# Kernel optimization log

Hardware: AMD Instinct MI355X
Metric: run time of the kernel (lower is better)

Reference implementation:

```python
import math
import jax, jax.numpy as jnp
import numpy as np
from jax import lax

MUL = 16           # multiplicity of 0e and 1o in input and output irreps
NRB = 8            # num_radial_basis
DIAMETER = 3.0
STEPS = (1.0, 1.0, 1.0)
DIM = 4 * MUL      # 16 scalars + 16 vectors * 3 = 64 channels


def _constants():
    # lattice from __init__: arange(-s, s+1) * step per axis, s = floor(r/step)
    r = DIAMETER / 2
    axes = [np.arange(-math.floor(r / st), math.floor(r / st) + 1.0) * st for st in STEPS]
    lattice = np.stack(np.meshgrid(*axes, indexing='ij'), axis=-1)  # [Kx,Ky,Kz,3]
    d = np.linalg.norm(lattice, axis=-1)                            # [Kx,Ky,Kz]
    # soft_one_hot_linspace(basis='smooth_finite', cutoff=True)
    values = np.linspace(0.0, r, NRB + 2)[1:-1]
    step = values[1] - values[0]
    diff = (d[..., None] - values) / step
    inside = diff ** 2 < 1.0
    emb = np.where(inside, 1.14136 * np.exp(2.0) * np.exp(-2.0 / np.where(inside, 1.0 - diff ** 2, 1.0)), 0.0)
    # spherical harmonics, normalize=True, normalization='component'
    n = lattice / np.maximum(d[..., None], 1e-12)  # unit vectors; 0 at the origin voxel
    sh0 = np.ones_like(d)                          # Y_0 (component normalized)
    sh1 = np.sqrt(3.0) * n                         # Y_1 (component normalized)
    return emb.astype(np.float32), sh0.astype(np.float32), sh1.astype(np.float32)

EMB, SH0, SH1 = _constants()
KX, KY, KZ = SH0.shape  # 3,3,3


def setup_inputs() -> dict:
    key = jax.random.key(0)
    ks = jax.random.split(key, 7)
    B, G = 4, 32
    return {
        'x': jax.random.normal(ks[0], (B, G, G, G, DIM), jnp.float32),
        'W_sc0': jax.random.normal(ks[1], (MUL, MUL), jnp.float32),  # Linear 0e->0e
        'W_sc1': jax.random.normal(ks[2], (MUL, MUL), jnp.float32),  # Linear 1o->1o
        'w1': jax.random.normal(ks[3], (NRB, MUL, MUL), jnp.float32),  # path 0e x 0e -> 0e
        'w2': jax.random.normal(ks[4], (NRB, MUL, MUL), jnp.float32),  # path 0e x 1o -> 1o
        'w3': jax.random.normal(ks[5], (NRB, MUL, MUL), jnp.float32),  # path 1o x 0e -> 1o
        'w4': jax.random.normal(ks[6], (NRB, MUL, MUL), jnp.float32),  # path 1o x 1o -> 0e
    }


def _kernel(w1, w2, w3, w4):
    # radial basis -> per-voxel path weights, divided by kernel volume (as in source)
    emb, sh0, sh1 = jnp.asarray(EMB), jnp.asarray(SH0), jnp.asarray(SH1)
    norm = float(KX * KY * KZ)
    W1, W2, W3, W4 = [jnp.einsum('xyzk,kio->xyzio', emb, w) / norm for w in (w1, w2, w3, w4)]
    # path normalization: each output irrep receives 2 paths of fan_in mul*1 = 16 -> 1/sqrt(32)
    alpha = 1.0 / np.sqrt(2.0 * MUL)
    # tp.right blocks (Clebsch-Gordan contractions, lmax=1):
    k00 = alpha * W1 * sh0[..., None, None]                                              # [.,i,o]
    k01 = alpha * jnp.einsum('xyzio,xyzm->xyziom', W2, sh1).reshape(KX, KY, KZ, MUL, 3 * MUL)
    k10 = (alpha / np.sqrt(3.0)) * jnp.einsum('xyzio,xyzm->xyzimo', W4, sh1).reshape(KX, KY, KZ, 3 * MUL, MUL)
    k11 = alpha * jnp.einsum('xyzio,mn->xyzimon', W3 * sh0[..., None, None],
                             jnp.eye(3, dtype=W3.dtype)).reshape(KX, KY, KZ, 3 * MUL, 3 * MUL)
    return jnp.concatenate([jnp.concatenate([k00, k01], axis=-1),
                            jnp.concatenate([k10, k11], axis=-1)], axis=-2)  # [Kx,Ky,Kz,64,64]


def reference(x, W_sc0, W_sc1, w1, w2, w3, w4):
    B, X, Y, Z, _ = x.shape
    inv_sqrt_mul = 1.0 / np.sqrt(MUL)
    # self-connection: e3nn Linear per irrep (applied pointwise over b,x,y,z)
    xs = x[..., :MUL]                                   # [B,X,Y,Z,16] scalars
    xv = x[..., MUL:].reshape(B, X, Y, Z, MUL, 3)       # [B,X,Y,Z,16,3] vectors
    sc_s = (xs @ W_sc0) * inv_sqrt_mul
    sc_v = jnp.einsum('bxyzic,io->bxyzoc', xv, W_sc1) * inv_sqrt_mul
    sc = jnp.concatenate([sc_s, sc_v.reshape(B, X, Y, Z, 3 * MUL)], axis=-1)
    # position-dependent equivariant kernel + standard 3D conv
    k = _kernel(w1, w2, w3, w4)
    conv = lax.conv_general_dilated(x, k, (1, 1, 1), 'SAME',
                                    dimension_numbers=('NXYZC', 'XYZIO', 'NXYZC'))
    return sc + conv
```

## Files before the change

### kernel.cpp

```cpp
#include <hip/hip_runtime.h>

typedef unsigned short u16;
typedef unsigned int u32;
typedef __bf16 bf16x8 __attribute__((ext_vector_type(8)));
typedef float f32x4 __attribute__((ext_vector_type(4)));
typedef u32 u32x4 __attribute__((ext_vector_type(4)));

#define AS1 __attribute__((address_space(1)))
#define AS3 __attribute__((address_space(3)))

__device__ __align__(16) u16 g_kT[27 * 64 * 64];
__device__ __align__(16) u16 g_kTr[27 * 8 * 512];

__device__ __forceinline__ u16 f2bf(float f) {
    unsigned int u = __float_as_uint(f);
    u += 0x7FFFu + ((u >> 16) & 1u);
    return (u16)(u >> 16);
}

__device__ __forceinline__ u32 pack_bf(float a, float b) {
    u32 ua = __float_as_uint(a) + 0x8000u;
    u32 ub = __float_as_uint(b) + 0x8000u;
    return __builtin_amdgcn_perm(ub, ua, 0x07060302u);
}

__global__ __launch_bounds__(256) void prep(
    const float* __restrict__ Wsc0, const float* __restrict__ Wsc1,
    const float* __restrict__ w1, const float* __restrict__ w2,
    const float* __restrict__ w3, const float* __restrict__ w4,
    const float* __restrict__ x, u16* __restrict__ xb, u32* __restrict__ zp)
{
    const int tid = threadIdx.x;
    if (blockIdx.x < 27) {
        if (tid >= 64) return;
        const int t = blockIdx.x;
        const int c = tid;
        const int dx = t / 9 - 1, dy = (t / 3) % 3 - 1, dz = t % 3 - 1;
        const float d = sqrtf((float)(dx * dx + dy * dy + dz * dz));
        const float step = 1.5f / 9.0f;
        float emb[8];
#pragma unroll
        for (int k = 0; k < 8; ++k) {
            float diff = (d - (float)(k + 1) * step) / step;
            float q = diff * diff;
            emb[k] = (q < 1.0f) ? 1.14136f * expf(2.0f - 2.0f / (1.0f - q)) : 0.0f;
        }
        const float dn = fmaxf(d, 1e-12f);
        const float s3 = 1.7320508075688772f;
        const float sh1[3] = { s3 * dx / dn, s3 * dy / dn, s3 * dz / dn };
        const float alpha  = 0.17677669529663687f;
        const float alpha3 = alpha * 0.57735026918962576f;

        u16* outp = &g_kT[(t * 64 + c) * 64];
        const int base2 = ((t * 2 + (c >> 5)) * 2 + ((c >> 4) & 1)) * 2;
        const int l15c  = c & 15;
        auto put = [&](int r, float v) {
            u16 h = f2bf(v);
            outp[r] = h;
            g_kTr[(base2 + (r >> 5)) * 512 + (((r >> 3) & 3) * 16 + l15c) * 8 + (r & 7)] = h;
        };

        if (c < 16) {
            const int o = c;
#pragma unroll
            for (int i = 0; i < 16; ++i) {
                float W1 = 0.f, W4 = 0.f;
#pragma unroll
                for (int k = 0; k < 8; ++k) {
                    W1 += emb[k] * w1[k * 256 + i * 16 + o];
                    W4 += emb[k] * w4[k * 256 + i * 16 + o];
                }
                W1 *= (1.0f / 27.0f); W4 *= (1.0f / 27.0f);
                float v0 = alpha * W1;
                if (t == 13) v0 += 0.25f * Wsc0[i * 16 + o];
                put(i, v0);
                const float base = alpha3 * W4;
#pragma unroll
                for (int m = 0; m < 3; ++m) put(16 + 3 * i + m, base * sh1[m]);
            }
        } else {
            const int o = (c - 16) / 3, nc = (c - 16) % 3;
#pragma unroll
            for (int i = 0; i < 16; ++i) {
                float W2 = 0.f, W3 = 0.f;
#pragma unroll
                for (int k = 0; k < 8; ++k) {
                    W2 += emb[k] * w2[k * 256 + i * 16 + o];
                    W3 += emb[k] * w3[k * 256 + i * 16 + o];
                }
                W2 *= (1.0f / 27.0f); W3 *= (1.0f / 27.0f);
                put(i, alpha * W2 * sh1[nc]);
#pragma unroll
                for (int m = 0; m < 3; ++m) {
                    float v = (m == nc) ? alpha * W3 : 0.0f;
                    if (t == 13 && m == nc) v += 0.25f * Wsc1[i * 16 + o];
                    put(16 + 3 * i + m, v);
                }
            }
        }
    } else {
        const int bid2 = blockIdx.x - 27;
        if (bid2 == 0) {
            u32x4 z = {0u, 0u, 0u, 0u};
            *reinterpret_cast<u32x4*>(zp + tid * 4) = z;
        }
        const size_t base = ((size_t)bid2 * 256 + tid) * 8;
        const float4* s = reinterpret_cast<const float4*>(x + base);
        float4 v0 = s[0], v1 = s[1];
        u32x4 p;
        p[0] = pack_bf(v0.x, v0.y); p[1] = pack_bf(v0.z, v0.w);
        p[2] = pack_bf(v1.x, v1.y); p[3] = pack_bf(v1.z, v1.w);
        *reinterpret_cast<u32x4*>(xb + base) = p;
    }
}

#define PLS 384
#define LDSB (3 * 48 * 1024)

#define ISSUE_B(s, t) \
  { const char* _p = bTr + (t) * 8192; \
    asm volatile("global_load_dwordx4 %0, %4, off\n\t" \
                 "global_load_dwordx4 %1, %4, off offset:1024\n\t" \
                 "global_load_dwordx4 %2, %4, off offset:2048\n\t" \
                 "global_load_dwordx4 %3, %4, off offset:3072" \
                 : "=&v"(B##s##0), "=&v"(B##s##1), "=&v"(B##s##2), "=&v"(B##s##3) \
                 : "v"(_p)); }

#define LOADA2(s, i0, i1, RCC) { \
  const int _r  = rbase + (RCC); \
  const int _o0 = _r * 128 + ((kg ^ (_r & 7)) << 4); \
  A##s##_##i0 = *reinterpret_cast<const bf16x8*>(abase + _o0); \
  A##s##_##i1 = *reinterpret_cast<const bf16x8*>(abase + (_o0 ^ 64)); }

#define RCC6(T, YY, MT) (((T)/9)*PLS + ((((T)/3)%3) + (YY))*34 + ((T)%3) + (MT)*16)

#define LOAD_A8(s, T) \
  LOADA2(s, 0, 1, RCC6(T,0,0)) \
  LOADA2(s, 2, 3, RCC6(T,0,1)) \
  LOADA2(s, 4, 5, RCC6(T,1,0)) \
  LOADA2(s, 6, 7, RCC6(T,1,1))

#define WAITV(N) \
  asm volatile("s_waitcnt vmcnt(" #N ")" ::: "memory"); \
  __builtin_amdgcn_sched_barrier(0);

#define BARRIER() \
  asm volatile("s_barrier" ::: "memory"); \
  __builtin_amdgcn_sched_barrier(0);

#define BC(x) __builtin_bit_cast(bf16x8, x)
#define MF(b_, a_, c_) __builtin_amdgcn_mfma_f32_16x16x32_bf16(BC(b_), a_, c_, 0, 0, 0)

#define MFMA16(bs, as) \
  acc000 = MF(B##bs##0, A##as##_0, acc000); acc001 = MF(B##bs##2, A##as##_0, acc001); \
  acc010 = MF(B##bs##0, A##as##_2, acc010); acc011 = MF(B##bs##2, A##as##_2, acc011); \
  acc100 = MF(B##bs##0, A##as##_4, acc100); acc101 = MF(B##bs##2, A##as##_4, acc101); \
  acc110 = MF(B##bs##0, A##as##_6, acc110); acc111 = MF(B##bs##2, A##as##_6, acc111); \
  acc000 = MF(B##bs##1, A##as##_1, acc000); acc001 = MF(B##bs##3, A##as##_1, acc001); \
  acc010 = MF(B##bs##1, A##as##_3, acc010); acc011 = MF(B##bs##3, A##as##_3, acc011); \
  acc100 = MF(B##bs##1, A##as##_5, acc100); acc101 = MF(B##bs##3, A##as##_5, acc101); \
  acc110 = MF(B##bs##1, A##as##_7, acc110); acc111 = MF(B##bs##3, A##as##_7, acc111);

__global__ __launch_bounds__(512, 2) void conv_mfma6(
    const u16* __restrict__ xb, const u32* __restrict__ zp,
    float* __restrict__ out)
{
    extern __shared__ u16 xt[];

    const int bid0 = blockIdx.x;
    const int bid  = (bid0 & 7) * 64 + (bid0 >> 3);
    const int b    = bid >> 7;
    const int X    = (bid >> 2) & 31;
    const int y0   = (bid & 3) << 3;
    const int tid  = threadIdx.x;
    const int wv   = tid >> 6;
    const int lane = tid & 63;
    const int l15  = lane & 15;
    const int kg   = lane >> 4;
    const int yh   = wv >> 1;
    const int nh   = wv & 1;

    const char* bTr = (const char*)g_kTr + nh * 4096 + lane * 16;

    u32x4 B00, B01, B02, B03, B10, B11, B12, B13, B20, B21, B22, B23,
          B30, B31, B32, B33, B40, B41, B42, B43;
    bf16x8 A0_0, A0_1, A0_2, A0_3, A0_4, A0_5, A0_6, A0_7;
    bf16x8 A1_0, A1_1, A1_2, A1_3, A1_4, A1_5, A1_6, A1_7;

    ISSUE_B(0, 1)
    ISSUE_B(1, 3)
    ISSUE_B(2, 4)
    ISSUE_B(3, 5)
    ISSUE_B(4, 7)

    {
        const int rloc = lane >> 3;
        const int swz  = (lane & 7) ^ rloc;
#pragma unroll
        for (int p = 0; p < 3; ++p) {
#pragma unroll
            for (int j = 0; j < 6; ++j) {
                const int cip = wv * 6 + j;
                const int c   = p * 48 + cip;
                const int rip = cip * 8 + rloc;
                const int yi  = rip / 34;
                const int zid = rip - yi * 34;
                const int xin = X + p - 1;
                const int yin = y0 + yi - 1;
                const int zin = zid - 1;
                const bool inb = (rip < 340) & ((unsigned)xin < 32u)
                               & ((unsigned)yin < 32u) & ((unsigned)zin < 32u);
                const u16* src = inb
                    ? xb + ((size_t)(((b * 32 + xin) * 32 + yin) * 32 + zin) * 64 + swz * 8)
                    : (const u16*)zp;
                __builtin_amdgcn_global_load_lds((const AS1 u32*)src,
                                                 (AS3 u32*)&xt[c * 512], 16, 0, 0);
            }
        }
    }

    const char* abase = reinterpret_cast<const char*>(xt);
    const int rbase = yh * 68 + l15;

    const f32x4 z4 = {0.f, 0.f, 0.f, 0.f};
    f32x4 acc000 = z4, acc001 = z4, acc010 = z4, acc011 = z4;
    f32x4 acc100 = z4, acc101 = z4, acc110 = z4, acc111 = z4;

    WAITV(12)
    BARRIER()
    LOAD_A8(0, 1)
    LOAD_A8(1, 3)   MFMA16(0, 0)
    LOAD_A8(0, 4)   MFMA16(1, 1)
    LOAD_A8(1, 5)   MFMA16(2, 0)
    LOAD_A8(0, 7)   MFMA16(3, 1)
                    MFMA16(4, 0)

    ISSUE_B(0, 9)
    ISSUE_B(1, 10)
    WAITV(4)
    BARRIER()
    LOAD_A8(1, 9)
    ISSUE_B(2, 11)  LOAD_A8(0, 10)            MFMA16(0, 1)
    ISSUE_B(0, 12)  LOAD_A8(1, 11)  WAITV(8)  MFMA16(1, 0)
    ISSUE_B(1, 13)  LOAD_A8(0, 12)  WAITV(8)  MFMA16(2, 1)
    ISSUE_B(2, 14)  LOAD_A8(1, 13)  WAITV(8)  MFMA16(0, 0)
    ISSUE_B(0, 15)  LOAD_A8(0, 14)  WAITV(8)  MFMA16(1, 1)
    ISSUE_B(1, 16)  LOAD_A8(1, 15)  WAITV(8)  MFMA16(2, 0)
    ISSUE_B(2, 17)  LOAD_A8(0, 16)  WAITV(8)  MFMA16(0, 1)
    ISSUE_B(0, 19)  LOAD_A8(1, 17)  WAITV(8)  MFMA16(1, 0)
    ISSUE_B(1, 21)  LOAD_A8(0, 19)  WAITV(8)  MFMA16(2, 1)
    ISSUE_B(2, 22)  LOAD_A8(1, 21)  WAITV(8)  MFMA16(0, 0)
    ISSUE_B(0, 23)  LOAD_A8(0, 22)  WAITV(8)  MFMA16(1, 1)
    ISSUE_B(1, 25)  LOAD_A8(1, 23)  WAITV(8)  MFMA16(2, 0)
                    LOAD_A8(0, 25)  WAITV(4)  MFMA16(0, 1)
                                    WAITV(0)  MFMA16(1, 0)

    float* obase = out + (((size_t)(b * 32 + X) * 32 + (y0 + yh * 2)) * 32) * 64
                 + nh * 32 + kg * 4;
    *reinterpret_cast<f32x4*>(obase + l15 * 64)                    = acc000;
    *reinterpret_cast<f32x4*>(obase + l15 * 64 + 16)               = acc001;
    *reinterpret_cast<f32x4*>(obase + (16 + l15) * 64)             = acc010;
    *reinterpret_cast<f32x4*>(obase + (16 + l15) * 64 + 16)        = acc011;
    *reinterpret_cast<f32x4*>(obase + 2048 + l15 * 64)             = acc100;
    *reinterpret_cast<f32x4*>(obase + 2048 + l15 * 64 + 16)        = acc101;
    *reinterpret_cast<f32x4*>(obase + 2048 + (16 + l15) * 64)      = acc110;
    *reinterpret_cast<f32x4*>(obase + 2048 + (16 + l15) * 64 + 16) = acc111;
}

#define ZS 68
#define NROWS 408

__global__ __launch_bounds__(256, 2) void conv_mfma_fb(
    const float* __restrict__ x, float* __restrict__ out)
{
    __shared__ __align__(16) u16 xts[NROWS * ZS];
    const int bid0 = blockIdx.x;
    const int bid  = (bid0 & 7) * 256 + (bid0 >> 3);
    const int b   = bid >> 9;
    const int X   = (bid >> 4) & 31;
    const int y0  = (bid & 15) << 1;
    const int tid = threadIdx.x;

    {
        const int pr = tid >> 2;
        const int q  = tid & 3;
#pragma unroll
        for (int pass = 0; pass < 7; ++pass) {
            const int idx = pass * 64 + pr;
            if (idx < NROWS) {
                const int rid = idx / 34;
                const int zid = idx - rid * 34;
                const int xin = X + (rid >> 2) - 1;
                const int yin = y0 + (rid & 3) - 1;
                const int zin = zid - 1;
                u32x4 p0 = {0u,0u,0u,0u}, p1 = {0u,0u,0u,0u};
                if ((unsigned)xin < 32u && (unsigned)yin < 32u && (unsigned)zin < 32u) {
                    const float4* src = reinterpret_cast<const float4*>(
                        x + ((((b * 32 + xin) * 32 + yin) * 32 + zin) * 64 + q * 16));
                    float4 v0 = src[0], v1 = src[1], v2 = src[2], v3 = src[3];
                    p0[0] = pack_bf(v0.x, v0.y); p0[1] = pack_bf(v0.z, v0.w);
                    p0[2] = pack_bf(v1.x, v1.y); p0[3] = pack_bf(v1.z, v1.w);
                    p1[0] = pack_bf(v2.x, v2.y); p1[1] = pack_bf(v2.z, v2.w);
                    p1[2] = pack_bf(v3.x, v3.y); p1[3] = pack_bf(v3.z, v3.w);
                }
                u16* dst = &xts[idx * ZS + q * 16];
                *reinterpret_cast<u32x4*>(dst)     = p0;
                *reinterpret_cast<u32x4*>(dst + 8) = p1;
            }
        }
    }
    __syncthreads();

    const int w    = tid >> 6;
    const int lane = tid & 63;
    const int l15  = lane & 15;
    const int kg   = lane >> 4;
    const int mh   = w >> 1;
    const int nh   = w & 1;
    const int chb  = kg * 8;

    const u16* abase = &xts[l15 * ZS + chb];
    const u16* bbase = &g_kT[(nh * 32 + l15) * 64 + chb];

    const f32x4 z4 = {0.f, 0.f, 0.f, 0.f};
    f32x4 acc[2][2] = {{z4, z4}, {z4, z4}};

    constexpr int NT = 19;
    constexpr int TAPS[NT] = {1,3,4,5,7,9,10,11,12,13,14,15,16,17,19,21,22,23,25};

#pragma unroll
    for (int ti = 0; ti < NT; ++ti) {
        const int t = TAPS[ti];
        const int dxt = t / 9, dyt = (t / 3) % 3, dzt = t % 3;
        const int rid = dxt * 4 + mh + dyt;
        bf16x8 bfr[4], afr[4];
#pragma unroll
        for (int kb = 0; kb < 2; ++kb)
#pragma unroll
        for (int nt = 0; nt < 2; ++nt)
            bfr[kb*2+nt] = *reinterpret_cast<const bf16x8*>(
                bbase + (t * 64 + nt * 16) * 64 + kb * 32);
#pragma unroll
        for (int kb = 0; kb < 2; ++kb)
#pragma unroll
        for (int mt = 0; mt < 2; ++mt)
            afr[kb*2+mt] = *reinterpret_cast<const bf16x8*>(
                abase + (rid * 34 + dzt + mt * 16) * ZS + kb * 32);
#pragma unroll
        for (int kb = 0; kb < 2; ++kb)
#pragma unroll
        for (int mt = 0; mt < 2; ++mt)
#pragma unroll
        for (int nt = 0; nt < 2; ++nt)
            acc[mt][nt] = __builtin_amdgcn_mfma_f32_16x16x32_bf16(
                bfr[kb*2+nt], afr[kb*2+mt], acc[mt][nt], 0, 0, 0);
    }

    float* obase = out + (((b * 32 + X) * 32 + (y0 + mh)) * 32) * 64 + nh * 32 + kg * 4;
#pragma unroll
    for (int mt = 0; mt < 2; ++mt)
#pragma unroll
        for (int nt = 0; nt < 2; ++nt) {
            float4 v;
            v.x = acc[mt][nt][0]; v.y = acc[mt][nt][1];
            v.z = acc[mt][nt][2]; v.w = acc[mt][nt][3];
            *reinterpret_cast<float4*>(obase + (mt * 16 + l15) * 64 + nt * 16) = v;
        }
}

extern "C" void kernel_launch(void* const* d_in, const int* in_sizes, int n_in,
                              void* d_out, int out_size, void* d_ws, size_t ws_size,
                              hipStream_t stream)
{
    const float* x    = (const float*)d_in[0];
    const float* Wsc0 = (const float*)d_in[1];
    const float* Wsc1 = (const float*)d_in[2];
    const float* w1   = (const float*)d_in[3];
    const float* w2   = (const float*)d_in[4];
    const float* w3   = (const float*)d_in[5];
    const float* w4   = (const float*)d_in[6];
    float* out = (float*)d_out;

    const size_t xb_bytes = (size_t)4 * 32 * 32 * 32 * 64 * 2;
    if (ws_size >= 4096 + xb_bytes) {
        u32* zp = (u32*)d_ws;
        u16* xb = (u16*)((char*)d_ws + 4096);
        prep<<<dim3(27 + 4096), dim3(256), 0, stream>>>(Wsc0, Wsc1, w1, w2, w3, w4,
                                                        x, xb, zp);
        conv_mfma6<<<dim3(512), dim3(512), LDSB, stream>>>(xb, zp, out);
    } else {
        prep<<<dim3(27), dim3(256), 0, stream>>>(Wsc0, Wsc1, w1, w2, w3, w4,
                                                 x, (u16*)nullptr, (u32*)nullptr);
        conv_mfma_fb<<<dim3(2048), dim3(256), 0, stream>>>(x, out);
    }
}
```

Measured before the change: 53.79 us.

## Shrink conv tile to 4x16 outputs with 256-thread blocks and more blocks

```diff
diff --git a/kernel.cpp b/kernel.cpp
--- a/kernel.cpp
+++ b/kernel.cpp
@@ -114,8 +114,7 @@
     }
 }
 
-#define PLS 384
-#define LDSB (3 * 48 * 1024)
+#define LDSW7 24576
 
 #define ISSUE_B(s, t) \
   { const char* _p = bTr + (t) * 8192; \
@@ -132,13 +131,11 @@
   A##s##_##i0 = *reinterpret_cast<const bf16x8*>(abase + _o0); \
   A##s##_##i1 = *reinterpret_cast<const bf16x8*>(abase + (_o0 ^ 64)); }
 
-#define RCC6(T, YY, MT) (((T)/9)*PLS + ((((T)/3)%3) + (YY))*34 + ((T)%3) + (MT)*16)
-
-#define LOAD_A8(s, T) \
-  LOADA2(s, 0, 1, RCC6(T,0,0)) \
-  LOADA2(s, 2, 3, RCC6(T,0,1)) \
-  LOADA2(s, 4, 5, RCC6(T,1,0)) \
-  LOADA2(s, 6, 7, RCC6(T,1,1))
+#define RCC7(T, YY) (((T)/9)*128 + ((((T)/3)%3) + (YY))*18 + ((T)%3))
+
+#define LOAD_A4(s, T) \
+  LOADA2(s, 0, 1, RCC7(T,0)) \
+  LOADA2(s, 2, 3, RCC7(T,1))
 
 #define WAITV(N) \
   asm volatile("s_waitcnt vmcnt(" #N ")" ::: "memory"); \
@@ -151,27 +148,26 @@
 #define BC(x) __builtin_bit_cast(bf16x8, x)
 #define MF(b_, a_, c_) __builtin_amdgcn_mfma_f32_16x16x32_bf16(BC(b_), a_, c_, 0, 0, 0)
 
-#define MFMA16(bs, as) \
-  acc000 = MF(B##bs##0, A##as##_0, acc000); acc001 = MF(B##bs##2, A##as##_0, acc001); \
-  acc010 = MF(B##bs##0, A##as##_2, acc010); acc011 = MF(B##bs##2, A##as##_2, acc011); \
-  acc100 = MF(B##bs##0, A##as##_4, acc100); acc101 = MF(B##bs##2, A##as##_4, acc101); \
-  acc110 = MF(B##bs##0, A##as##_6, acc110); acc111 = MF(B##bs##2, A##as##_6, acc111); \
-  acc000 = MF(B##bs##1, A##as##_1, acc000); acc001 = MF(B##bs##3, A##as##_1, acc001); \
-  acc010 = MF(B##bs##1, A##as##_3, acc010); acc011 = MF(B##bs##3, A##as##_3, acc011); \
-  acc100 = MF(B##bs##1, A##as##_5, acc100); acc101 = MF(B##bs##3, A##as##_5, acc101); \
-  acc110 = MF(B##bs##1, A##as##_7, acc110); acc111 = MF(B##bs##3, A##as##_7, acc111);
-
-__global__ __launch_bounds__(512, 2) void conv_mfma6(
+#define MFMA8(bs, as) \
+  acc00 = MF(B##bs##0, A##as##_0, acc00); acc01 = MF(B##bs##2, A##as##_0, acc01); \
+  acc10 = MF(B##bs##0, A##as##_2, acc10); acc11 = MF(B##bs##2, A##as##_2, acc11); \
+  acc00 = MF(B##bs##1, A##as##_1, acc00); acc01 = MF(B##bs##3, A##as##_1, acc01); \
+  acc10 = MF(B##bs##1, A##as##_3, acc10); acc11 = MF(B##bs##3, A##as##_3, acc11);
+
+__global__ __launch_bounds__(256, 3) void conv_mfma7(
     const u16* __restrict__ xb, const u32* __restrict__ zp,
     float* __restrict__ out)
 {
-    extern __shared__ u16 xt[];
+    __shared__ __align__(16) u16 xt[LDSW7];
 
     const int bid0 = blockIdx.x;
-    const int bid  = (bid0 & 7) * 64 + (bid0 >> 3);
-    const int b    = bid >> 7;
-    const int X    = (bid >> 2) & 31;
-    const int y0   = (bid & 3) << 3;
+    const int bid  = (bid0 & 7) * 256 + (bid0 >> 3);
+    const int b    = bid >> 9;
+    const int X    = (bid >> 4) & 31;
+    const int yg   = (bid >> 1) & 7;
+    const int zg   = bid & 1;
+    const int y0   = yg << 2;
+    const int z0   = zg << 4;
     const int tid  = threadIdx.x;
     const int wv   = tid >> 6;
     const int lane = tid & 63;
@@ -182,16 +178,12 @@
 
     const char* bTr = (const char*)g_kTr + nh * 4096 + lane * 16;
 
-    u32x4 B00, B01, B02, B03, B10, B11, B12, B13, B20, B21, B22, B23,
-          B30, B31, B32, B33, B40, B41, B42, B43;
-    bf16x8 A0_0, A0_1, A0_2, A0_3, A0_4, A0_5, A0_6, A0_7;
-    bf16x8 A1_0, A1_1, A1_2, A1_3, A1_4, A1_5, A1_6, A1_7;
+    u32x4 B00, B01, B02, B03, B10, B11, B12, B13, B20, B21, B22, B23;
+    bf16x8 A0_0, A0_1, A0_2, A0_3;
+    bf16x8 A1_0, A1_1, A1_2, A1_3;
 
     ISSUE_B(0, 1)
     ISSUE_B(1, 3)
-    ISSUE_B(2, 4)
-    ISSUE_B(3, 5)
-    ISSUE_B(4, 7)
 
     {
         const int rloc = lane >> 3;
@@ -199,72 +191,80 @@
 #pragma unroll
         for (int p = 0; p < 3; ++p) {
 #pragma unroll
-            for (int j = 0; j < 6; ++j) {
-                const int cip = wv * 6 + j;
-                const int c   = p * 48 + cip;
+            for (int j = 0; j < 4; ++j) {
+                const int cip = wv * 4 + j;
                 const int rip = cip * 8 + rloc;
-                const int yi  = rip / 34;
-                const int zid = rip - yi * 34;
+                const int yi  = rip / 18;
+                const int zid = rip - yi * 18;
                 const int xin = X + p - 1;
                 const int yin = y0 + yi - 1;
-                const int zin = zid - 1;
-                const bool inb = (rip < 340) & ((unsigned)xin < 32u)
+                const int zin = z0 + zid - 1;
+                const bool inb = (rip < 108) & ((unsigned)xin < 32u)
                                & ((unsigned)yin < 32u) & ((unsigned)zin < 32u);
                 const u16* src = inb
                     ? xb + ((size_t)(((b * 32 + xin) * 32 + yin) * 32 + zin) * 64 + swz * 8)
                     : (const u16*)zp;
                 __builtin_amdgcn_global_load_lds((const AS1 u32*)src,
-                                                 (AS3 u32*)&xt[c * 512], 16, 0, 0);
+                                                 (AS3 u32*)&xt[(p * 16 + cip) * 512],
+                                                 16, 0, 0);
             }
         }
     }
 
     const char* abase = reinterpret_cast<const char*>(xt);
-    const int rbase = yh * 68 + l15;
+    const int rbase = yh * 36 + l15;
 
     const f32x4 z4 = {0.f, 0.f, 0.f, 0.f};
-    f32x4 acc000 = z4, acc001 = z4, acc010 = z4, acc011 = z4;
-    f32x4 acc100 = z4, acc101 = z4, acc110 = z4, acc111 = z4;
-
-    WAITV(12)
+    f32x4 acc00 = z4, acc01 = z4, acc10 = z4, acc11 = z4;
+
+    WAITV(8)
     BARRIER()
-    LOAD_A8(0, 1)
-    LOAD_A8(1, 3)   MFMA16(0, 0)
-    LOAD_A8(0, 4)   MFMA16(1, 1)
-    LOAD_A8(1, 5)   MFMA16(2, 0)
-    LOAD_A8(0, 7)   MFMA16(3, 1)
-                    MFMA16(4, 0)
-
-    ISSUE_B(0, 9)
-    ISSUE_B(1, 10)
-    WAITV(4)
+
+    LOAD_A4(0, 1)
+    ISSUE_B(2, 4)
+    LOAD_A4(1, 3)            MFMA8(0, 0)
+    ISSUE_B(0, 5)
+    LOAD_A4(0, 4)            MFMA8(1, 1)
+    ISSUE_B(1, 7)
+    LOAD_A4(1, 5)  WAITV(8)  MFMA8(2, 0)
+    ISSUE_B(2, 9)
     BARRIER()
-    LOAD_A8(1, 9)
-    ISSUE_B(2, 11)  LOAD_A8(0, 10)            MFMA16(0, 1)
-    ISSUE_B(0, 12)  LOAD_A8(1, 11)  WAITV(8)  MFMA16(1, 0)
-    ISSUE_B(1, 13)  LOAD_A8(0, 12)  WAITV(8)  MFMA16(2, 1)
-    ISSUE_B(2, 14)  LOAD_A8(1, 13)  WAITV(8)  MFMA16(0, 0)
-    ISSUE_B(0, 15)  LOAD_A8(0, 14)  WAITV(8)  MFMA16(1, 1)
-    ISSUE_B(1, 16)  LOAD_A8(1, 15)  WAITV(8)  MFMA16(2, 0)
-    ISSUE_B(2, 17)  LOAD_A8(0, 16)  WAITV(8)  MFMA16(0, 1)
-    ISSUE_B(0, 19)  LOAD_A8(1, 17)  WAITV(8)  MFMA16(1, 0)
-    ISSUE_B(1, 21)  LOAD_A8(0, 19)  WAITV(8)  MFMA16(2, 1)
-    ISSUE_B(2, 22)  LOAD_A8(1, 21)  WAITV(8)  MFMA16(0, 0)
-    ISSUE_B(0, 23)  LOAD_A8(0, 22)  WAITV(8)  MFMA16(1, 1)
-    ISSUE_B(1, 25)  LOAD_A8(1, 23)  WAITV(8)  MFMA16(2, 0)
-                    LOAD_A8(0, 25)  WAITV(4)  MFMA16(0, 1)
-                                    WAITV(0)  MFMA16(1, 0)
-
-    float* obase = out + (((size_t)(b * 32 + X) * 32 + (y0 + yh * 2)) * 32) * 64
+    LOAD_A4(0, 7)  WAITV(8)  MFMA8(0, 1)
+    ISSUE_B(0, 10)
+    LOAD_A4(1, 9)  WAITV(8)  MFMA8(1, 0)
+    ISSUE_B(1, 11)
+    LOAD_A4(0, 10) WAITV(8)  MFMA8(2, 1)
+    ISSUE_B(2, 12)
+    LOAD_A4(1, 11) WAITV(8)  MFMA8(0, 0)
+    ISSUE_B(0, 13)
+    LOAD_A4(0, 12) WAITV(8)  MFMA8(1, 1)
+    ISSUE_B(1, 14)
+    LOAD_A4(1, 13) WAITV(8)  MFMA8(2, 0)
+    ISSUE_B(2, 15)
+    LOAD_A4(0, 14) WAITV(8)  MFMA8(0, 1)
+    ISSUE_B(0, 16)
+    LOAD_A4(1, 15) WAITV(8)  MFMA8(1, 0)
+    ISSUE_B(1, 17)
+    LOAD_A4(0, 16) WAITV(8)  MFMA8(2, 1)
+    ISSUE_B(2, 19)
+    LOAD_A4(1, 17) WAITV(8)  MFMA8(0, 0)
+    ISSUE_B(0, 21)
+    LOAD_A4(0, 19) WAITV(8)  MFMA8(1, 1)
+    ISSUE_B(1, 22)
+    LOAD_A4(1, 21) WAITV(8)  MFMA8(2, 0)
+    ISSUE_B(2, 23)
+    LOAD_A4(0, 22) WAITV(8)  MFMA8(0, 1)
+    ISSUE_B(0, 25)
+    LOAD_A4(1, 23) WAITV(8)  MFMA8(1, 0)
+    LOAD_A4(0, 25) WAITV(4)  MFMA8(2, 1)
+                   WAITV(0)  MFMA8(0, 0)
+
+    float* obase = out + ((((size_t)(b * 32 + X) * 32 + (y0 + yh * 2)) * 32) + z0) * 64
                  + nh * 32 + kg * 4;
-    *reinterpret_cast<f32x4*>(obase + l15 * 64)                    = acc000;
-    *reinterpret_cast<f32x4*>(obase + l15 * 64 + 16)               = acc001;
-    *reinterpret_cast<f32x4*>(obase + (16 + l15) * 64)             = acc010;
-    *reinterpret_cast<f32x4*>(obase + (16 + l15) * 64 + 16)        = acc011;
-    *reinterpret_cast<f32x4*>(obase + 2048 + l15 * 64)             = acc100;
-    *reinterpret_cast<f32x4*>(obase + 2048 + l15 * 64 + 16)        = acc101;
-    *reinterpret_cast<f32x4*>(obase + 2048 + (16 + l15) * 64)      = acc110;
-    *reinterpret_cast<f32x4*>(obase + 2048 + (16 + l15) * 64 + 16) = acc111;
+    *reinterpret_cast<f32x4*>(obase + l15 * 64)               = acc00;
+    *reinterpret_cast<f32x4*>(obase + l15 * 64 + 16)          = acc01;
+    *reinterpret_cast<f32x4*>(obase + 2048 + l15 * 64)        = acc10;
+    *reinterpret_cast<f32x4*>(obase + 2048 + l15 * 64 + 16)   = acc11;
 }
 
 #define ZS 68
@@ -387,7 +387,7 @@
         u16* xb = (u16*)((char*)d_ws + 4096);
         prep<<<dim3(27 + 4096), dim3(256), 0, stream>>>(Wsc0, Wsc1, w1, w2, w3, w4,
                                                         x, xb, zp);
-        conv_mfma6<<<dim3(512), dim3(512), LDSB, stream>>>(xb, zp, out);
+        conv_mfma7<<<dim3(2048), dim3(256), 0, stream>>>(xb, zp, out);
     } else {
         prep<<<dim3(27), dim3(256), 0, stream>>>(Wsc0, Wsc1, w1, w2, w3, w4,
                                                  x, (u16*)nullptr, (u32*)nullptr);
```

Result: slower. 56.33 us (+4.7%).
